# Optimization experiments

Hardware: AMD Instinct MI355X
Metric: run time of the kernel (lower is better)

## Reference

```python
import jax, jax.numpy as jnp
import numpy as np

HEADS = 20  # SDXL-style: hidden_size 1280 / head_dim 64
IP_SCALE = 1.0


def setup_inputs() -> dict:
    key = jax.random.key(0)
    ks = jax.random.split(key, 12)
    B, Sq, T, C, D, NIP = 4, 4096, 77, 1280, 2048, 16
    s = lambda fan: 1.0 / np.sqrt(fan)
    # post-softmax multiplicative mask: col 0 (sot token) forced to 1, rest a binary spatial mask
    spat = (jax.random.uniform(ks[0], (1, Sq, 1)) < 0.5).astype(jnp.float32)
    attention_mask = jnp.concatenate([jnp.ones((1, Sq, 1)), jnp.tile(spat, (1, 1, T - 1))], axis=-1)
    return {
        "hidden_states": jax.random.normal(ks[1], (B, Sq, C), jnp.float32),
        "encoder_hidden_states": jax.random.normal(ks[2], (B, T, D), jnp.float32),
        "ip_hidden_states": jax.random.normal(ks[3], (B, NIP, D), jnp.float32),
        "attention_mask": attention_mask,
        "Wq": jax.random.normal(ks[4], (C, C), jnp.float32) * s(C),
        "Wk": jax.random.normal(ks[5], (D, C), jnp.float32) * s(D),
        "Wv": jax.random.normal(ks[6], (D, C), jnp.float32) * s(D),
        "Wo": jax.random.normal(ks[7], (C, C), jnp.float32) * s(C),
        "bo": jnp.zeros((C,), jnp.float32),
        "Wk_ip": jax.random.normal(ks[8], (D, C), jnp.float32) * s(D),
        "Wv_ip": jax.random.normal(ks[9], (D, C), jnp.float32) * s(D),
    }


def reference(hidden_states, encoder_hidden_states, ip_hidden_states, attention_mask,
              Wq, Wk, Wv, Wo, bo, Wk_ip, Wv_ip):
    B, Sq, C = hidden_states.shape
    H = HEADS
    d = C // H
    scale = d ** -0.5
    # projections (torch Linear with weights stored [in, out])
    q = (hidden_states @ Wq).reshape(B, Sq, H, d)
    k = (encoder_hidden_states @ Wk).reshape(B, -1, H, d)
    v = (encoder_hidden_states @ Wv).reshape(B, -1, H, d)
    # explicit QK^T softmax, then POST-softmax multiplicative mask (as in get_attention_scores + mask multiply)
    scores = jnp.einsum('bqhd,bkhd->bhqk', q, k) * scale
    probs = jax.nn.softmax(scores, axis=-1)
    probs = probs * attention_mask[:, None, :, :]  # [1,1,Sq,T] broadcast over batch*heads
    out = jnp.einsum('bhqk,bkhd->bqhd', probs, v).reshape(B, Sq, C)
    out = out @ Wo + bo  # to_out[0]; to_out[1] is dropout (identity at eval)
    # IP-adapter stream (single stream, no spatial ip mask): standard SDPA against ip tokens
    k_ip = (ip_hidden_states @ Wk_ip).reshape(B, -1, H, d)
    v_ip = (ip_hidden_states @ Wv_ip).reshape(B, -1, H, d)
    s_ip = jnp.einsum('bqhd,bkhd->bhqk', q, k_ip) * scale
    p_ip = jax.nn.softmax(s_ip, axis=-1)
    ip_out = jnp.einsum('bhqk,bkhd->bqhd', p_ip, v_ip).reshape(B, Sq, C)
    return out + IP_SCALE * ip_out
```

## Files before the change

### kernel.cpp

```cpp
#include <hip/hip_runtime.h>

typedef __attribute__((ext_vector_type(4))) float f32x4;
typedef __attribute__((ext_vector_type(8))) short s16x8;
typedef __attribute__((ext_vector_type(8))) __bf16 bf16x8;
typedef unsigned short u16;

__device__ __forceinline__ u16 f2b(float f) {
  union { float f; unsigned u; } x; x.f = f;
  unsigned r = x.u + 0x7fffu + ((x.u >> 16) & 1u);
  return (u16)(r >> 16);
}
__device__ __forceinline__ float b2f(u16 u) {
  union { unsigned u; float f; } x; x.u = ((unsigned)u) << 16;
  return x.f;
}
__device__ __forceinline__ void gld16(const void* g, void* l) {
  __builtin_amdgcn_global_load_lds(
      (const __attribute__((address_space(1))) unsigned int*)g,
      (__attribute__((address_space(3))) unsigned int*)l, 16, 0, 0);
}
__device__ __forceinline__ f32x4 mfma_bf16(s16x8 a, s16x8 b, f32x4 c) {
  return __builtin_amdgcn_mfma_f32_16x16x32_bf16(
      __builtin_bit_cast(bf16x8, a), __builtin_bit_cast(bf16x8, b), c, 0, 0, 0);
}

#define BAR() asm volatile("s_barrier" ::: "memory")

__global__ void k_convert_all(const float* __restrict__ hs, const float* __restrict__ ehs,
                              const float* __restrict__ iph,
                              u16* __restrict__ hsb, u16* __restrict__ ehsb,
                              u16* __restrict__ ipb) {
  const int n1 = 16384 * 1280 / 4, n2 = 308 * 2048 / 4, n3 = 64 * 2048 / 4;
  int i = blockIdx.x * blockDim.x + threadIdx.x;
  const float* src; u16* dst; int j = i;
  if (i < n1) { src = hs; dst = hsb; }
  else if (i < n1 + n2) { src = ehs; dst = ehsb; j = i - n1; }
  else if (i < n1 + n2 + n3) { src = iph; dst = ipb; j = i - n1 - n2; }
  else return;
  float4 v = ((const float4*)src)[j];
  ushort4 o;
  o.x = f2b(v.x); o.y = f2b(v.y); o.z = f2b(v.z); o.w = f2b(v.w);
  ((ushort4*)dst)[j] = o;
}

__global__ void k_transpose_all(const float* Wk, const float* Wv, const float* Wkip,
                                const float* Wvip, const float* Wq, const float* Wo,
                                u16* TK, u16* TV, u16* TKip, u16* TVip,
                                u16* TQ, u16* TO) {
  const int z = blockIdx.z;
  const float* W = (z == 0) ? Wk : (z == 1) ? Wv : (z == 2) ? Wkip
                  : (z == 3) ? Wvip : (z == 4) ? Wq : Wo;
  u16* T = (z == 0) ? TK : (z == 1) ? TV : (z == 2) ? TKip
          : (z == 3) ? TVip : (z == 4) ? TQ : TO;
  const int K = (z < 4) ? 2048 : 1280;
  const int N = 1280;
  __shared__ float tile[32][33];
  int n0 = blockIdx.x * 32, k0 = blockIdx.y * 32;
  if (k0 >= K) return;
  int tx = threadIdx.x & 31, ty = threadIdx.x >> 5;
#pragma unroll
  for (int i = 0; i < 32; i += 8)
    tile[ty + i][tx] = W[(size_t)(k0 + ty + i) * N + n0 + tx];
  __syncthreads();
#pragma unroll
  for (int i = 0; i < 32; i += 8)
    T[(size_t)(n0 + ty + i) * K + k0 + tx] = f2b(tile[tx][ty + i]);
}

__device__ __forceinline__ void gemm_core0(
    const u16* __restrict__ A, const u16* __restrict__ BT,
    int M, int N, int K, u16* __restrict__ outb, int m0, int n0) {
  const int tid = threadIdx.x;
  const int l = tid & 63;
  const int w = tid >> 6;
  const int wr = w >> 1, wc = w & 1;
  __shared__ u16 As[128 * 32];
  __shared__ u16 Bs[128 * 32];
  f32x4 acc[4][4] = {};

  const int o0 = tid * 16;
  const int o1 = o0 + 4096;
  const int ra0 = o0 >> 6, ca0 = (o0 & 63) >> 1;
  const int ra1 = o1 >> 6, ca1 = (o1 & 63) >> 1;
  int ga0 = m0 + ra0; if (ga0 >= M) ga0 = M - 1;
  int ga1 = m0 + ra1; if (ga1 >= M) ga1 = M - 1;
  const u16* Ar0 = A + (size_t)ga0 * K + ca0;
  const u16* Ar1 = A + (size_t)ga1 * K + ca1;
  const u16* Br0 = BT + (size_t)(n0 + ra0) * K + ca0;
  const u16* Br1 = BT + (size_t)(n0 + ra1) * K + ca1;

  for (int k0 = 0; k0 < K; k0 += 32) {
    gld16(Ar0 + k0, &As[o0 >> 1]);
    gld16(Ar1 + k0, &As[o1 >> 1]);
    gld16(Br0 + k0, &Bs[o0 >> 1]);
    gld16(Br1 + k0, &Bs[o1 >> 1]);
    __syncthreads();
    s16x8 af[4], bfr[4];
#pragma unroll
    for (int mi = 0; mi < 4; ++mi)
      af[mi] = *(const s16x8*)&As[(wr * 64 + mi * 16 + (l & 15)) * 32 + (l >> 4) * 8];
#pragma unroll
    for (int ni = 0; ni < 4; ++ni)
      bfr[ni] = *(const s16x8*)&Bs[(wc * 64 + ni * 16 + (l & 15)) * 32 + (l >> 4) * 8];
#pragma unroll
    for (int mi = 0; mi < 4; ++mi)
#pragma unroll
      for (int ni = 0; ni < 4; ++ni)
        acc[mi][ni] = mfma_bf16(af[mi], bfr[ni], acc[mi][ni]);
    __syncthreads();
  }

#pragma unroll
  for (int mi = 0; mi < 4; ++mi) {
    const int mbase = m0 + wr * 64 + mi * 16 + (l >> 4) * 4;
#pragma unroll
    for (int ni = 0; ni < 4; ++ni) {
      const int ncol = n0 + wc * 64 + ni * 16 + (l & 15);
#pragma unroll
      for (int r = 0; r < 4; ++r) {
        int m = mbase + r;
        if (m < M) outb[(size_t)m * N + ncol] = f2b(acc[mi][ni][r]);
      }
    }
  }
}

__global__ __launch_bounds__(256) void k_gemm_small4(
    const u16* __restrict__ ehsb, const u16* __restrict__ ipb,
    const u16* __restrict__ WkT, const u16* __restrict__ WvT,
    const u16* __restrict__ WkipT, const u16* __restrict__ WvipT,
    u16* kbuf, u16* vbuf, u16* kipb, u16* vipb) {
  const int z = blockIdx.z;
  const int M = (z < 2) ? 308 : 64;
  const int m0 = blockIdx.y * 128;
  if (m0 >= M) return;
  const u16* A = (z < 2) ? ehsb : ipb;
  const u16* BT = (z == 0) ? WkT : (z == 1) ? WvT : (z == 2) ? WkipT : WvipT;
  u16* out = (z == 0) ? kbuf : (z == 1) ? vbuf : (z == 2) ? kipb : vipb;
  gemm_core0(A, BT, M, 1280, 2048, out, m0, blockIdx.x * 128);
}

template <int EPI>
__global__ __launch_bounds__(512, 4) void k_gemm128(
    const u16* __restrict__ A, const u16* __restrict__ BT,
    int N, int K, float alpha,
    u16* __restrict__ outb, float* __restrict__ outf,
    const float* __restrict__ bias, const u16* __restrict__ ipadd,
    int nbx) {
  __shared__ u16 lds[28672];
  const int tid = threadIdx.x, l = tid & 63, w = tid >> 6;
  const int lr = l & 15, lg = l >> 4;
  const int wr = w >> 2, wc = w & 3;

  const int nwg = gridDim.x;
  const int q = nwg >> 3, r = nwg & 7;
  const int xcd = blockIdx.x & 7, lid = blockIdx.x >> 3;
  const int wg = (xcd < r) ? (xcd * (q + 1) + lid)
                           : (r * (q + 1) + (xcd - r) * q + lid);
  const int bm0 = (wg / nbx) * 128, bn0 = (wg % nbx) * 320;

  const int rA = tid >> 2;
  const int rB1 = (tid + 512) >> 2;
  const int rB2 = (tid + 1024) >> 2;
  const int sl0 = ((tid & 3) ^ ((rA >> 1) & 3)) * 8;
  const int sl1 = ((tid & 3) ^ ((rB1 >> 1) & 3)) * 8;
  const int sl2 = ((tid & 3) ^ ((rB2 >> 1) & 3)) * 8;
  const int aOff = (bm0 + rA) * K + sl0;
  const int bOff0 = (bn0 + rA) * K + sl0;
  const int bOff1 = (bn0 + rB1) * K + sl1;
  const int bOff2 = (bn0 + rB2) * K + sl2;
  const int dA = tid * 8;
  const int dB0 = 4096 + tid * 8;
  const int dB1 = 4096 + (tid + 512) * 8;
  const int dB2 = 4096 + (tid + 1024) * 8;
  const bool wlo = (tid < 256);

  const int KT = K >> 5;
  f32x4 acc[4][5] = {};

  const int xsw = (lg ^ ((lr >> 1) & 3)) * 8;
  const int aR = (wr * 64 + lr) * 32 + xsw;
  const int bR = 4096 + (wc * 80 + lr) * 32 + xsw;

#define VM0() asm volatile("s_waitcnt vmcnt(0)" ::: "memory")
#define STAGE(s, kt)                                                   \
  {                                                                    \
    const int sb_ = (s) * 14336;                                       \
    const int ko_ = (kt) * 32;                                         \
    gld16(A + aOff + ko_, &lds[sb_ + dA]);                             \
    gld16(BT + bOff0 + ko_, &lds[sb_ + dB0]);                          \
    gld16(BT + bOff1 + ko_, &lds[sb_ + dB1]);                          \
    if (wlo) gld16(BT + bOff2 + ko_, &lds[sb_ + dB2]);                 \
  }

  STAGE(0, 0);
  VM0();
  BAR();

  for (int j = 0; j < KT; ++j) {
    const int sb = (j & 1) * 14336;
    const bool pf = (j + 1 < KT);
    if (pf) STAGE((j + 1) & 1, j + 1);
    s16x8 afv[4];
#pragma unroll
    for (int mi = 0; mi < 4; ++mi)
      afv[mi] = *(const s16x8*)&lds[sb + aR + mi * 512];
#pragma unroll
    for (int ni = 0; ni < 5; ++ni) {
      s16x8 bfv = *(const s16x8*)&lds[sb + bR + ni * 512];
      __builtin_amdgcn_s_setprio(1);
#pragma unroll
      for (int mi = 0; mi < 4; ++mi)
        acc[mi][ni] = mfma_bf16(afv[mi], bfv, acc[mi][ni]);
      __builtin_amdgcn_s_setprio(0);
    }
    VM0();
    BAR();
  }

  __syncthreads();

  if constexpr (EPI == 0) {
#pragma unroll
    for (int half = 0; half < 2; ++half) {
      if (half) __syncthreads();
      if (wr == half) {
#pragma unroll
        for (int mi = 0; mi < 4; ++mi) {
          const int row = mi * 16 + lg * 4;
#pragma unroll
          for (int ni = 0; ni < 5; ++ni) {
            const int col = wc * 80 + ni * 16 + lr;
#pragma unroll
            for (int rr = 0; rr < 4; ++rr)
              lds[(row + rr) * 320 + col] = f2b(acc[mi][ni][rr] * alpha);
          }
        }
      }
      __syncthreads();
      const int rbase = tid >> 3;
      const int cseg = tid & 7;
#pragma unroll
      for (int jj = 0; jj < 5; ++jj) {
        const int ch = cseg + jj * 8;
        *(int4*)(outb + (size_t)(bm0 + half * 64 + rbase) * N + bn0 + ch * 8) =
            *(const int4*)&lds[rbase * 320 + ch * 8];
      }
    }
  } else {
#pragma unroll
    for (int mi = 0; mi < 4; ++mi) {
      const int mrow = bm0 + wr * 64 + mi * 16 + lg * 4;
#pragma unroll
      for (int ni = 0; ni < 5; ++ni) {
        const int ncol = bn0 + wc * 80 + ni * 16 + lr;
#pragma unroll
        for (int rr = 0; rr < 4; ++rr) {
          const size_t idx = (size_t)(mrow + rr) * N + ncol;
          outf[idx] = acc[mi][ni][rr] + bias[ncol] + b2f(ipadd[idx]);
        }
      }
    }
  }
#undef VM0
#undef STAGE
}

__global__ __launch_bounds__(512, 4) void k_attn(
    const u16* __restrict__ Q,
    const u16* __restrict__ Kb,
    const u16* __restrict__ Vb,
    const u16* __restrict__ Kip,
    const u16* __restrict__ Vip,
    const float* __restrict__ mask,
    u16* __restrict__ Oattn,
    u16* __restrict__ Oip) {
  const int qt = blockIdx.x, h = blockIdx.y, b = blockIdx.z;
  const int tid = threadIdx.x, l = tid & 63, w = tid >> 6;
  const int lr = l & 15, lg = l >> 4;
  const int r0 = w * 16;
  const int m0 = b * 4096 + qt * 128;

  __shared__ u16 KV[192][72];
  __shared__ u16 Ps[128][104];
  __shared__ u16 P2s[128][40];

  const u16* qrow = Q + (size_t)(m0 + r0 + lr) * 1280 + h * 64;
  s16x8 aq0 = *(const s16x8*)(qrow + lg * 8);
  s16x8 aq1 = *(const s16x8*)(qrow + 32 + lg * 8);

  for (int s = tid; s < 192 * 8; s += 512) {
    const int row = s >> 3, seg = s & 7;
    int4 v = {0, 0, 0, 0};
    const u16* src = nullptr;
    if (row < 77)       src = Kb  + (size_t)(b * 77 + row) * 1280 + h * 64 + seg * 8;
    else if (row < 80)  src = nullptr;
    else if (row < 96)  src = Kip + (size_t)(b * 16 + row - 80) * 1280 + h * 64 + seg * 8;
    else if (row < 173) src = Vb  + (size_t)(b * 77 + row - 96) * 1280 + h * 64 + seg * 8;
    else if (row < 176) src = nullptr;
    else                src = Vip + (size_t)(b * 16 + row - 176) * 1280 + h * 64 + seg * 8;
    if (src) v = *(const int4*)src;
    *(int4*)&KV[row][(seg ^ ((row >> 3) & 3)) * 8] = v;
  }
  __syncthreads();

  f32x4 sc[5];
  f32x4 sip = {};
#pragma unroll
  for (int t5 = 0; t5 < 6; ++t5) {
    const int trow = t5 * 16 + lr;
    const int qz = (trow >> 3) & 3;
    s16x8 b0 = *(const s16x8*)&KV[trow][(lg ^ qz) * 8];
    s16x8 b1 = *(const s16x8*)&KV[trow][((lg + 4) ^ qz) * 8];
    f32x4 c = {};
    c = mfma_bf16(aq0, b0, c);
    c = mfma_bf16(aq1, b1, c);
    if (t5 < 5) sc[t5] = c; else sip = c;
  }

#pragma unroll
  for (int r = 0; r < 4; ++r) {
    float mx = fmaxf(fmaxf(fmaxf(sc[0][r], sc[1][r]), fmaxf(sc[2][r], sc[3][r])), sc[4][r]);
    mx = fmaxf(mx, __shfl_xor(mx, 1));
    mx = fmaxf(mx, __shfl_xor(mx, 2));
    mx = fmaxf(mx, __shfl_xor(mx, 4));
    mx = fmaxf(mx, __shfl_xor(mx, 8));
    float p[5], sm = 0.f;
#pragma unroll
    for (int t5 = 0; t5 < 5; ++t5) {
      bool valid = (t5 < 4) | (lr < 13);
      p[t5] = valid ? __expf(sc[t5][r] - mx) : 0.f;
      sm += p[t5];
    }
    sm += __shfl_xor(sm, 1);
    sm += __shfl_xor(sm, 2);
    sm += __shfl_xor(sm, 4);
    sm += __shfl_xor(sm, 8);
    const float inv = 1.0f / sm;
    const int row = r0 + lg * 4 + r;
    const int qg = qt * 128 + row;
#pragma unroll
    for (int t5 = 0; t5 < 5; ++t5) {
      int t = t5 * 16 + lr;
      float pf = 0.f;
      if (t < 77) pf = p[t5] * inv * mask[qg * 77 + t];
      Ps[row][t] = f2b(pf);
    }
    Ps[row][80 + lr] = 0;

    float m2 = sip[r];
    m2 = fmaxf(m2, __shfl_xor(m2, 1));
    m2 = fmaxf(m2, __shfl_xor(m2, 2));
    m2 = fmaxf(m2, __shfl_xor(m2, 4));
    m2 = fmaxf(m2, __shfl_xor(m2, 8));
    float pi = __expf(sip[r] - m2);
    float s2 = pi;
    s2 += __shfl_xor(s2, 1);
    s2 += __shfl_xor(s2, 2);
    s2 += __shfl_xor(s2, 4);
    s2 += __shfl_xor(s2, 8);
    P2s[row][lr] = 0;
    P2s[row][16 + lr] = f2b(pi / s2);
  }

  s16x8 ap[3];
#pragma unroll
  for (int ks = 0; ks < 3; ++ks)
    ap[ks] = *(const s16x8*)&Ps[r0 + lr][ks * 32 + lg * 8];
  s16x8 aip = *(const s16x8*)&P2s[r0 + lr][lg * 8];

  f32x4 om[4], oi[4];
#pragma unroll
  for (int nt = 0; nt < 4; ++nt) {
    const int dcol = (nt * 16 + lr) ^ (lg << 3);
    f32x4 o = {};
#pragma unroll
    for (int ks = 0; ks < 3; ++ks) {
      s16x8 bv;
#pragma unroll
      for (int j = 0; j < 8; ++j)
        bv[j] = (short)KV[96 + ks * 32 + lg * 8 + j][dcol];
      o = mfma_bf16(ap[ks], bv, o);
    }
    s16x8 bip;
#pragma unroll
    for (int j = 0; j < 8; ++j)
      bip[j] = (short)KV[160 + lg * 8 + j][dcol];
    f32x4 o2 = {};
    o2 = mfma_bf16(aip, bip, o2);
    om[nt] = o;
    oi[nt] = o2;
  }

  __syncthreads();

  u16 (*Om)[72] = (u16(*)[72]) & KV[0][0];
  u16 (*Oi)[72] = (u16(*)[72]) & Ps[0][0];
#pragma unroll
  for (int nt = 0; nt < 4; ++nt)
#pragma unroll
    for (int r = 0; r < 4; ++r) {
      const int row = r0 + lg * 4 + r;
      const int d = nt * 16 + lr;
      Om[row][d] = f2b(om[nt][r]);
      Oi[row][d] = f2b(oi[nt][r]);
    }
  __syncthreads();

  for (int s = tid; s < 128 * 8; s += 512) {
    const int row = s >> 3, seg = s & 7;
    const size_t g = (size_t)(m0 + row) * 1280 + h * 64 + seg * 8;
    *(int4*)(Oattn + g) = *(const int4*)&Om[row][seg * 8];
    *(int4*)(Oip + g) = *(const int4*)&Oi[row][seg * 8];
  }
}

extern "C" void kernel_launch(void* const* d_in, const int* in_sizes, int n_in,
                              void* d_out, int out_size, void* d_ws, size_t ws_size,
                              hipStream_t stream) {
  (void)in_sizes; (void)n_in; (void)out_size; (void)ws_size;
  const float* hs   = (const float*)d_in[0];
  const float* ehs  = (const float*)d_in[1];
  const float* iph  = (const float*)d_in[2];
  const float* mask = (const float*)d_in[3];
  const float* Wq   = (const float*)d_in[4];
  const float* Wk   = (const float*)d_in[5];
  const float* Wv   = (const float*)d_in[6];
  const float* Wo   = (const float*)d_in[7];
  const float* bo   = (const float*)d_in[8];
  const float* Wkip = (const float*)d_in[9];
  const float* Wvip = (const float*)d_in[10];
  float* out = (float*)d_out;

  char* ws = (char*)d_ws;
  size_t off = 0;
  auto alloc = [&](size_t bytes) {
    char* p = ws + off;
    off += (bytes + 255) & ~(size_t)255;
    return p;
  };
  u16* hsb   = (u16*)alloc(16384ull * 1280 * 2);
  u16* qbuf  = (u16*)alloc(16384ull * 1280 * 2);
  u16* ipout = (u16*)alloc(16384ull * 1280 * 2);
  u16* WqT   = (u16*)alloc(1280ull * 1280 * 2);
  u16* WoT   = (u16*)alloc(1280ull * 1280 * 2);
  u16* WkT   = (u16*)alloc(1280ull * 2048 * 2);
  u16* WvT   = (u16*)alloc(1280ull * 2048 * 2);
  u16* WkipT = (u16*)alloc(1280ull * 2048 * 2);
  u16* WvipT = (u16*)alloc(1280ull * 2048 * 2);
  u16* ehsb  = (u16*)alloc(308ull * 2048 * 2);
  u16* ipb   = (u16*)alloc(64ull * 2048 * 2);
  u16* kbuf  = (u16*)alloc(308ull * 1280 * 2);
  u16* vbuf  = (u16*)alloc(308ull * 1280 * 2);
  u16* kipb  = (u16*)alloc(64ull * 1280 * 2);
  u16* vipb  = (u16*)alloc(64ull * 1280 * 2);

  const int ntot4 = (16384 * 1280 + 308 * 2048 + 64 * 2048) / 4;
  k_convert_all<<<(ntot4 + 255) / 256, 256, 0, stream>>>(hs, ehs, iph, hsb, ehsb, ipb);
  k_transpose_all<<<dim3(40, 64, 6), 256, 0, stream>>>(Wk, Wv, Wkip, Wvip, Wq, Wo,
                                                       WkT, WvT, WkipT, WvipT, WqT, WoT);

  k_gemm128<0><<<512, 512, 0, stream>>>(hsb, WqT, 1280, 1280, 0.125f,
                                        qbuf, nullptr, nullptr, nullptr, 4);
  k_gemm_small4<<<dim3(10, 3, 4), 256, 0, stream>>>(ehsb, ipb, WkT, WvT, WkipT, WvipT,
                                                    kbuf, vbuf, kipb, vipb);

  k_attn<<<dim3(32, 20, 4), 512, 0, stream>>>(qbuf, kbuf, vbuf, kipb, vipb, mask,
                                              hsb, ipout);

  k_gemm128<1><<<512, 512, 0, stream>>>(hsb, WoT, 1280, 1280, 1.f,
                                        nullptr, out, bo, ipout, 4);
}
```

Measured before the change: 271.2 us.

## Fuse fp32-to-bf16 conversion of hidden states into Q GEMM, triple-buffer small GEMM

The Q projection GEMM now reads fp32 hidden states directly, converting them to bf16 in registers and writing them to LDS. This removes the separate conversion pass over the large 16384x1280 activation tensor and its bf16 round trip through memory. The small K/V GEMM core also moves from a single LDS buffer to a three-stage pipeline using vmcnt waits, so loads overlap compute. The trade-off is that the Q GEMM loads A through registers instead of direct global-to-LDS copies, which adds register pressure and some latency exposure.

After: 281.9 us. +4.0%, slower.

```diff
diff --git a/kernel.cpp b/kernel.cpp
--- a/kernel.cpp
+++ b/kernel.cpp
@@ -26,16 +26,13 @@
 
 #define BAR() asm volatile("s_barrier" ::: "memory")
 
-__global__ void k_convert_all(const float* __restrict__ hs, const float* __restrict__ ehs,
-                              const float* __restrict__ iph,
-                              u16* __restrict__ hsb, u16* __restrict__ ehsb,
-                              u16* __restrict__ ipb) {
-  const int n1 = 16384 * 1280 / 4, n2 = 308 * 2048 / 4, n3 = 64 * 2048 / 4;
+__global__ void k_convert_small(const float* __restrict__ ehs, const float* __restrict__ iph,
+                                u16* __restrict__ ehsb, u16* __restrict__ ipb) {
+  const int n2 = 308 * 2048 / 4, n3 = 64 * 2048 / 4;
   int i = blockIdx.x * blockDim.x + threadIdx.x;
   const float* src; u16* dst; int j = i;
-  if (i < n1) { src = hs; dst = hsb; }
-  else if (i < n1 + n2) { src = ehs; dst = ehsb; j = i - n1; }
-  else if (i < n1 + n2 + n3) { src = iph; dst = ipb; j = i - n1 - n2; }
+  if (i < n2) { src = ehs; dst = ehsb; }
+  else if (i < n2 + n3) { src = iph; dst = ipb; j = i - n2; }
   else return;
   float4 v = ((const float4*)src)[j];
   ushort4 o;
@@ -74,8 +71,8 @@
   const int l = tid & 63;
   const int w = tid >> 6;
   const int wr = w >> 1, wc = w & 1;
-  __shared__ u16 As[128 * 32];
-  __shared__ u16 Bs[128 * 32];
+  __shared__ u16 As[3][128 * 32];
+  __shared__ u16 Bs[3][128 * 32];
   f32x4 acc[4][4] = {};
 
   const int o0 = tid * 16;
@@ -89,25 +86,43 @@
   const u16* Br0 = BT + (size_t)(n0 + ra0) * K + ca0;
   const u16* Br1 = BT + (size_t)(n0 + ra1) * K + ca1;
 
-  for (int k0 = 0; k0 < K; k0 += 32) {
-    gld16(Ar0 + k0, &As[o0 >> 1]);
-    gld16(Ar1 + k0, &As[o1 >> 1]);
-    gld16(Br0 + k0, &Bs[o0 >> 1]);
-    gld16(Br1 + k0, &Bs[o1 >> 1]);
-    __syncthreads();
+  const int KT = K >> 5;
+#define SSTAGE(s, kt)                                 \
+  {                                                   \
+    const int k0_ = (kt) << 5;                        \
+    gld16(Ar0 + k0_, &As[s][o0 >> 1]);                \
+    gld16(Ar1 + k0_, &As[s][o1 >> 1]);                \
+    gld16(Br0 + k0_, &Bs[s][o0 >> 1]);                \
+    gld16(Br1 + k0_, &Bs[s][o1 >> 1]);                \
+  }
+  SSTAGE(0, 0);
+  SSTAGE(1, 1);
+  asm volatile("s_waitcnt vmcnt(4)" ::: "memory");
+  BAR();
+
+  int slot = 0;
+  for (int j = 0; j < KT; ++j) {
+    const bool pf = (j + 2 < KT);
+    if (pf) {
+      int s2 = slot + 2; if (s2 >= 3) s2 -= 3;
+      SSTAGE(s2, j + 2);
+    }
     s16x8 af[4], bfr[4];
 #pragma unroll
     for (int mi = 0; mi < 4; ++mi)
-      af[mi] = *(const s16x8*)&As[(wr * 64 + mi * 16 + (l & 15)) * 32 + (l >> 4) * 8];
+      af[mi] = *(const s16x8*)&As[slot][(wr * 64 + mi * 16 + (l & 15)) * 32 + (l >> 4) * 8];
 #pragma unroll
     for (int ni = 0; ni < 4; ++ni)
-      bfr[ni] = *(const s16x8*)&Bs[(wc * 64 + ni * 16 + (l & 15)) * 32 + (l >> 4) * 8];
+      bfr[ni] = *(const s16x8*)&Bs[slot][(wc * 64 + ni * 16 + (l & 15)) * 32 + (l >> 4) * 8];
 #pragma unroll
     for (int mi = 0; mi < 4; ++mi)
 #pragma unroll
       for (int ni = 0; ni < 4; ++ni)
         acc[mi][ni] = mfma_bf16(af[mi], bfr[ni], acc[mi][ni]);
-    __syncthreads();
+    if (pf) asm volatile("s_waitcnt vmcnt(4)" ::: "memory");
+    else    asm volatile("s_waitcnt vmcnt(0)" ::: "memory");
+    BAR();
+    ++slot; if (slot >= 3) slot = 0;
   }
 
 #pragma unroll
@@ -123,6 +138,7 @@
       }
     }
   }
+#undef SSTAGE
 }
 
 __global__ __launch_bounds__(256) void k_gemm_small4(
@@ -142,8 +158,8 @@
 
 template <int EPI>
 __global__ __launch_bounds__(512, 4) void k_gemm128(
-    const u16* __restrict__ A, const u16* __restrict__ BT,
-    int N, int K, float alpha,
+    const float* __restrict__ Af, const u16* __restrict__ Ab,
+    const u16* __restrict__ BT, int N, int K, float alpha,
     u16* __restrict__ outb, float* __restrict__ outf,
     const float* __restrict__ bias, const u16* __restrict__ ipadd,
     int nbx) {
@@ -183,24 +199,53 @@
   const int bR = 4096 + (wc * 80 + lr) * 32 + xsw;
 
 #define VM0() asm volatile("s_waitcnt vmcnt(0)" ::: "memory")
-#define STAGE(s, kt)                                                   \
+#define LGKM0() asm volatile("s_waitcnt lgkmcnt(0)" ::: "memory")
+#define STAGE_B(s, kt)                                                 \
   {                                                                    \
     const int sb_ = (s) * 14336;                                       \
     const int ko_ = (kt) * 32;                                         \
-    gld16(A + aOff + ko_, &lds[sb_ + dA]);                             \
     gld16(BT + bOff0 + ko_, &lds[sb_ + dB0]);                          \
     gld16(BT + bOff1 + ko_, &lds[sb_ + dB1]);                          \
     if (wlo) gld16(BT + bOff2 + ko_, &lds[sb_ + dB2]);                 \
   }
-
-  STAGE(0, 0);
+#define CVT_WRITE_A(s, v0, v1)                                         \
+  {                                                                    \
+    bf16x8 pk_;                                                        \
+    pk_[0] = (__bf16)(v0).x; pk_[1] = (__bf16)(v0).y;                  \
+    pk_[2] = (__bf16)(v0).z; pk_[3] = (__bf16)(v0).w;                  \
+    pk_[4] = (__bf16)(v1).x; pk_[5] = (__bf16)(v1).y;                  \
+    pk_[6] = (__bf16)(v1).z; pk_[7] = (__bf16)(v1).w;                  \
+    *(s16x8*)&lds[(s) * 14336 + dA] = __builtin_bit_cast(s16x8, pk_);  \
+  }
+
+  if constexpr (EPI == 0) {
+    float4 v0 = *(const float4*)(Af + aOff);
+    float4 v1 = *(const float4*)(Af + aOff + 4);
+    STAGE_B(0, 0);
+    CVT_WRITE_A(0, v0, v1);
+    LGKM0();
+  } else {
+    gld16(Ab + aOff, &lds[dA]);
+    STAGE_B(0, 0);
+  }
   VM0();
   BAR();
 
   for (int j = 0; j < KT; ++j) {
     const int sb = (j & 1) * 14336;
+    const int ns = (j & 1) ^ 1;
     const bool pf = (j + 1 < KT);
-    if (pf) STAGE((j + 1) & 1, j + 1);
+    float4 va0, va1;
+    if (pf) {
+      const int ko = (j + 1) * 32;
+      if constexpr (EPI == 0) {
+        va0 = *(const float4*)(Af + aOff + ko);
+        va1 = *(const float4*)(Af + aOff + ko + 4);
+      } else {
+        gld16(Ab + aOff + ko, &lds[ns * 14336 + dA]);
+      }
+      STAGE_B(ns, j + 1);
+    }
     s16x8 afv[4];
 #pragma unroll
     for (int mi = 0; mi < 4; ++mi)
@@ -215,6 +260,12 @@
       __builtin_amdgcn_s_setprio(0);
     }
     VM0();
+    if (pf) {
+      if constexpr (EPI == 0) {
+        CVT_WRITE_A(ns, va0, va1);
+        LGKM0();
+      }
+    }
     BAR();
   }
 
@@ -263,7 +314,9 @@
     }
   }
 #undef VM0
-#undef STAGE
+#undef LGKM0
+#undef STAGE_B
+#undef CVT_WRITE_A
 }
 
 __global__ __launch_bounds__(512, 4) void k_attn(
@@ -455,12 +508,12 @@
   u16* kipb  = (u16*)alloc(64ull * 1280 * 2);
   u16* vipb  = (u16*)alloc(64ull * 1280 * 2);
 
-  const int ntot4 = (16384 * 1280 + 308 * 2048 + 64 * 2048) / 4;
-  k_convert_all<<<(ntot4 + 255) / 256, 256, 0, stream>>>(hs, ehs, iph, hsb, ehsb, ipb);
+  const int nsm4 = (308 * 2048 + 64 * 2048) / 4;
+  k_convert_small<<<(nsm4 + 255) / 256, 256, 0, stream>>>(ehs, iph, ehsb, ipb);
   k_transpose_all<<<dim3(40, 64, 6), 256, 0, stream>>>(Wk, Wv, Wkip, Wvip, Wq, Wo,
                                                        WkT, WvT, WkipT, WvipT, WqT, WoT);
 
-  k_gemm128<0><<<512, 512, 0, stream>>>(hsb, WqT, 1280, 1280, 0.125f,
+  k_gemm128<0><<<512, 512, 0, stream>>>(hs, nullptr, WqT, 1280, 1280, 0.125f,
                                         qbuf, nullptr, nullptr, nullptr, 4);
   k_gemm_small4<<<dim3(10, 3, 4), 256, 0, stream>>>(ehsb, ipb, WkT, WvT, WkipT, WvipT,
                                                     kbuf, vbuf, kipb, vipb);
@@ -468,6 +521,6 @@
   k_attn<<<dim3(32, 20, 4), 512, 0, stream>>>(qbuf, kbuf, vbuf, kipb, vipb, mask,
                                               hsb, ipout);
 
-  k_gemm128<1><<<512, 512, 0, stream>>>(hsb, WoT, 1280, 1280, 1.f,
+  k_gemm128<1><<<512, 512, 0, stream>>>(nullptr, hsb, WoT, 1280, 1280, 1.f,
                                         nullptr, out, bo, ipout, 4);
 }
```
